# Kernel optimization log

Measured on AMD Instinct MI355X. Metric: run time of the kernel, lower is better.

The kernel has to match this reference:

```python
import jax, jax.numpy as jnp
import numpy as np

N = 40000      # nodes
E = 640000     # edges (avg degree 16)
F_IN = 15      # in_node_nf
F_EDGE = 4     # in_edge_nf
H = 128        # hidden_nf
L = 4          # n_layers
OUT = 21       # graph_dec output (hardcoded in module)


def setup_inputs() -> dict:
    key = jax.random.key(0)
    ks = jax.random.split(key, 16)
    def rn(k, shape, s=0.02):
        return jax.random.normal(k, shape, dtype=jnp.float32) * s
    e_in = 2 * H + 1 + F_EDGE   # edge_mlp input width: src,tgt,radial,edge_attr
    n_in = 2 * H + F_IN         # node_mlp input width: h, agg, node_attr(h0)
    return {
        "h0": jax.random.normal(ks[0], (N, F_IN), dtype=jnp.float32),
        "x": jax.random.normal(ks[1], (N, 3), dtype=jnp.float32),
        "edges": jax.random.randint(ks[2], (2, E), 0, N, dtype=jnp.int32),
        "edge_attr": jax.random.normal(ks[3], (E, F_EDGE), dtype=jnp.float32),
        "emb_w": rn(ks[4], (F_IN, H)), "emb_b": jnp.zeros((H,), jnp.float32),
        "ew1": rn(ks[5], (L, e_in, H)), "eb1": jnp.zeros((L, H), jnp.float32),
        "ew2": rn(ks[6], (L, H, H)), "eb2": jnp.zeros((L, H), jnp.float32),
        "nw1": rn(ks[7], (L, n_in, H)), "nb1": jnp.zeros((L, H), jnp.float32),
        "nw2": rn(ks[8], (L, H, H)), "nb2": jnp.zeros((L, H), jnp.float32),
        "dw1": rn(ks[9], (H, H)), "db1": jnp.zeros((H,), jnp.float32),
        "dw2": rn(ks[10], (H, H)), "db2": jnp.zeros((H,), jnp.float32),
        "gw1": rn(ks[11], (H, H)), "gb1": jnp.zeros((H,), jnp.float32),
        "gw2": rn(ks[12], (H, OUT)), "gb2": jnp.zeros((OUT,), jnp.float32),
    }


def reference(h0, x, edges, edge_attr, emb_w, emb_b, ew1, eb1, ew2, eb2,
              nw1, nb1, nw2, nb2, dw1, db1, dw2, db2, gw1, gb1, gw2, gb2):
    silu = jax.nn.silu
    row, col = edges[0], edges[1]
    # coord2radial (coords are constant across layers; coord_model is never called)
    cd = x[row] - x[col]                                  # [E,3]
    radial = jnp.sum(cd * cd, axis=-1, keepdims=True)     # [E,1]
    h = h0 @ emb_w + emb_b                                # [N,H]
    for i in range(L):
        # edge_model: cat(h[row], h[col], radial, edge_attr) -> MLP (act on both layers)
        ein = jnp.concatenate([h[row], h[col], radial, edge_attr], axis=-1)
        ef = silu(ein @ ew1[i] + eb1[i])
        ef = silu(ef @ ew2[i] + eb2[i])                   # [E,H]
        # node_model: scatter-sum messages to row nodes, concat, MLP, residual
        agg = jax.ops.segment_sum(ef, row, num_segments=h.shape[0])  # [N,H]
        nin = jnp.concatenate([h, agg, h0], axis=-1)
        h = h + (silu(nin @ nw1[i] + nb1[i]) @ nw2[i] + nb2[i])
    # node_dec then graph_dec (per-node prediction of 21 values)
    h = silu(h @ dw1 + db1) @ dw2 + db2
    pred = silu(h @ gw1 + gb1) @ gw2 + gb2                # [N,21]
    return pred
```

## Files before the change

### kernel.cpp

```cpp
#include <hip/hip_runtime.h>
#include <hip/hip_bf16.h>
#include <math.h>

#define N_NODES 40000
#define N_EDGES 640000
#define F_IN    15
#define HID     128
#define NLAYERS 4
#define NOUT    21

#define FLAG_BIAS 1
#define FLAG_ACC  2
#define FLAG_SILU 4

typedef __attribute__((ext_vector_type(8))) short bf16x8;
typedef __attribute__((ext_vector_type(16))) float f32x16;
typedef __attribute__((ext_vector_type(2)))  float vf2;

__device__ __forceinline__ float silu_f(float x) {
    return x * __builtin_amdgcn_rcpf(1.0f + __expf(-x));
}

__device__ __forceinline__ unsigned short f2bf(float f) {
    unsigned u = __builtin_bit_cast(unsigned, f);
    unsigned r = (u + 0x7FFFu + ((u >> 16) & 1u)) >> 16;
    return (unsigned short)r;
}
__device__ __forceinline__ float bf2f(unsigned short b) {
    return __builtin_bit_cast(float, (unsigned)b << 16);
}

__device__ __forceinline__ void split2v(vf2 v, unsigned& hi2, unsigned& lo2) {
    union { __hip_bfloat162 b; unsigned u; } ch, cl;
    ch.b = __float22bfloat162_rn(make_float2(v.x, v.y));
    vf2 h;
    h.x = __builtin_bit_cast(float, ch.u << 16);
    h.y = __builtin_bit_cast(float, ch.u & 0xFFFF0000u);
    vf2 r = v - h;
    cl.b = __float22bfloat162_rn(make_float2(r.x, r.y));
    hi2 = ch.u;
    lo2 = cl.u;
}

__device__ __forceinline__ void store_split(char* a_hi, char* a_lo, int row, int col, float v) {
    unsigned short h = f2bf(v);
    unsigned short l = f2bf(v - bf2f(h));
    int byte = (row * 256 + col * 2) ^ ((row & 7) << 4);
    *(unsigned short*)(a_hi + byte) = h;
    *(unsigned short*)(a_lo + byte) = l;
}

__global__ __launch_bounds__(256) void radial_kernel(
    const float* __restrict__ x, const int* __restrict__ erow,
    const int* __restrict__ ecol, float* __restrict__ radial)
{
    int e = blockIdx.x * 256 + threadIdx.x;
    if (e >= N_EDGES) return;
    int r = erow[e], c = ecol[e];
    float dx = x[r*3+0] - x[c*3+0];
    float dy = x[r*3+1] - x[c*3+1];
    float dz = x[r*3+2] - x[c*3+2];
    radial[e] = dx*dx + dy*dy + dz*dz;
}

__global__ __launch_bounds__(256) void hist_kernel(
    const int* __restrict__ erow, int* __restrict__ cnt)
{
    int e = blockIdx.x * 256 + threadIdx.x;
    if (e < N_EDGES) atomicAdd(&cnt[erow[e]], 1);
}

__global__ __launch_bounds__(1024) void scan_kernel(
    const int* __restrict__ cnt, int* __restrict__ rowptr)
{
    __shared__ int s[1024];
    __shared__ int carry_s;
    const int tid = threadIdx.x;
    if (tid == 0) { carry_s = 0; rowptr[0] = 0; }
    __syncthreads();
    for (int base = 0; base < N_NODES; base += 1024) {
        int i = base + tid;
        int v = (i < N_NODES) ? cnt[i] : 0;
        s[tid] = v;
        __syncthreads();
        for (int off = 1; off < 1024; off <<= 1) {
            int t = (tid >= off) ? s[tid - off] : 0;
            __syncthreads();
            s[tid] += t;
            __syncthreads();
        }
        int c = carry_s;
        if (i < N_NODES) rowptr[i + 1] = c + s[tid];
        __syncthreads();
        if (tid == 1023) carry_s = c + s[1023];
        __syncthreads();
    }
}

__global__ __launch_bounds__(256) void scatter_kernel(
    const int* __restrict__ erow, const int* __restrict__ ecol,
    const float* __restrict__ radial, const float* __restrict__ edge_attr,
    const int* __restrict__ rowptr, int* __restrict__ fill,
    int* __restrict__ srow, int* __restrict__ scol,
    float* __restrict__ srad, float* __restrict__ sea)
{
    int e = blockIdx.x * 256 + threadIdx.x;
    if (e >= N_EDGES) return;
    int r = erow[e];
    int pos = rowptr[r] + atomicAdd(&fill[r], 1);
    srow[pos] = r;
    scol[pos] = ecol[e];
    srad[pos] = radial[e];
    float4 ea = *(const float4*)&edge_attr[(size_t)e * 4];
    *(float4*)&sea[(size_t)pos * 4] = ea;
}

#define OFF_W2   0
#define OFF_W1A  65536
#define OFF_W1B  131072
#define OFF_NW1  196608
#define OFF_NW2  335872
#define OFF_DW1  401408
#define OFF_DW2  417792
#define OFF_GW1  434176
#define W_TOTAL  450560

__global__ __launch_bounds__(256) void prep_all_kernel(
    const float* __restrict__ ew1, const float* __restrict__ ew2,
    const float* __restrict__ nw1, const float* __restrict__ nw2,
    const float* __restrict__ dw1, const float* __restrict__ dw2,
    const float* __restrict__ gw1,
    unsigned short* __restrict__ hi, unsigned short* __restrict__ lo)
{
    const int T = blockIdx.y;
    int srcSel, srcOff, K, dstOff;
    if (T < 4)       { srcSel=1; srcOff=T*16384;           K=128; dstOff=OFF_W2 +T*16384; }
    else if (T < 8)  { int l=T-4;  srcSel=0; srcOff=l*33408;        K=128; dstOff=OFF_W1A+l*16384; }
    else if (T < 12) { int l=T-8;  srcSel=0; srcOff=l*33408+16384;  K=128; dstOff=OFF_W1B+l*16384; }
    else if (T < 16) { int l=T-12; srcSel=2; srcOff=l*34688;        K=271; dstOff=OFF_NW1+l*34816; }
    else if (T < 20) { int l=T-16; srcSel=3; srcOff=l*16384;        K=128; dstOff=OFF_NW2+l*16384; }
    else if (T == 20){ srcSel=4; srcOff=0; K=128; dstOff=OFF_DW1; }
    else if (T == 21){ srcSel=5; srcOff=0; K=128; dstOff=OFF_DW2; }
    else             { srcSel=6; srcOff=0; K=128; dstOff=OFF_GW1; }

    const float* src;
    switch (srcSel) {
        case 0: src = ew1; break;  case 1: src = ew2; break;
        case 2: src = nw1; break;  case 3: src = nw2; break;
        case 4: src = dw1; break;  case 5: src = dw2; break;
        default: src = gw1; break;
    }
    int K16 = (K + 15) & ~15;
    int idx = blockIdx.x * 256 + threadIdx.x;
    if (idx >= K16 * 128) return;
    int k = idx >> 7, c = idx & 127;
    float v = (k < K) ? src[srcOff + k * 128 + c] : 0.0f;
    unsigned short h = f2bf(v);
    unsigned short lw = f2bf(v - bf2f(h));
    int o = dstOff + ((k >> 3) << 10) + (c << 3) + (k & 7);
    hi[o] = h; lo[o] = lw;
}

__global__ __launch_bounds__(256) void gemm_kernel(
    const float* __restrict__ A, int lda,
    const float* __restrict__ W, int ldw,
    const float* __restrict__ bias,
    float* __restrict__ out, int ldout,
    int M, int K, int J, int flags)
{
    __shared__ float s_a[32 * 132];
    const int tid = threadIdx.x;
    const int row0 = blockIdx.x * 32;

    for (int idx = tid; idx < 32 * K; idx += 256) {
        int r = (K == 128) ? (idx >> 7) : (idx / K);
        int k = idx - r * K;
        int gr = row0 + r;
        s_a[r * 132 + k] = (gr < M) ? A[(size_t)gr * lda + k] : 0.0f;
    }
    __syncthreads();

    const int jg = tid & 31;
    const int rg = tid >> 5;
    const int j  = jg * 4;
    const int r0 = rg * 4;

    float acc[4][4] = {};

    if (j < J) {
        const bool w4ok = ((ldw & 3) == 0) && (j + 4 <= J);
        int k = 0;
        for (; k + 4 <= K; k += 4) {
            float4 av[4];
            #pragma unroll
            for (int i = 0; i < 4; i++)
                av[i] = *(const float4*)&s_a[(r0 + i) * 132 + k];
            #pragma unroll
            for (int kk = 0; kk < 4; kk++) {
                const float* wp = W + (size_t)(k + kk) * ldw + j;
                float4 w4;
                if (w4ok) {
                    w4 = *(const float4*)wp;
                } else {
                    w4.x = (j + 0 < J) ? wp[0] : 0.0f;
                    w4.y = (j + 1 < J) ? wp[1] : 0.0f;
                    w4.z = (j + 2 < J) ? wp[2] : 0.0f;
                    w4.w = (j + 3 < J) ? wp[3] : 0.0f;
                }
                #pragma unroll
                for (int i = 0; i < 4; i++) {
                    float a = ((const float*)&av[i])[kk];
                    acc[i][0] += a * w4.x;
                    acc[i][1] += a * w4.y;
                    acc[i][2] += a * w4.z;
                    acc[i][3] += a * w4.w;
                }
            }
        }
        for (; k < K; k++) {
            const float* wp = W + (size_t)k * ldw + j;
            float w0 = (j + 0 < J) ? wp[0] : 0.0f;
            float w1 = (j + 1 < J) ? wp[1] : 0.0f;
            float w2 = (j + 2 < J) ? wp[2] : 0.0f;
            float w3 = (j + 3 < J) ? wp[3] : 0.0f;
            #pragma unroll
            for (int i = 0; i < 4; i++) {
                float a = s_a[(r0 + i) * 132 + k];
                acc[i][0] += a * w0;
                acc[i][1] += a * w1;
                acc[i][2] += a * w2;
                acc[i][3] += a * w3;
            }
        }
    }

    #pragma unroll
    for (int i = 0; i < 4; i++) {
        int gr = row0 + r0 + i;
        if (gr >= M) continue;
        #pragma unroll
        for (int t = 0; t < 4; t++) {
            int jj = j + t;
            if (jj >= J) continue;
            float v = acc[i][t];
            if (flags & FLAG_BIAS) v += bias[jj];
            if (flags & FLAG_ACC)  v += out[(size_t)gr * ldout + jj];
            if (flags & FLAG_SILU) v = silu_f(v);
            out[(size_t)gr * ldout + jj] = v;
        }
    }
}

__device__ __forceinline__ void stage_a_chunk(
    char* a_hi, char* a_lo,
    const float* __restrict__ A1, int lda1, int KA1,
    const float* __restrict__ A2, int lda2, int KA,
    int kc, int row0, int lane, int w)
{
    if (kc + 128 <= KA1) {
        #pragma unroll 4
        for (int it = 0; it < 16; ++it) {
            int row = it * 4 + w;
            vf2 v = *(const vf2*)&A1[(size_t)(row0 + row) * lda1 + kc + lane * 2];
            unsigned hi2, lo2;
            split2v(v, hi2, lo2);
            int byte = (row * 256 + lane * 4) ^ ((row & 7) << 4);
            *(unsigned*)(a_hi + byte) = hi2;
            *(unsigned*)(a_lo + byte) = lo2;
        }
    } else {
        for (int it = 0; it < 16; ++it) {
            int row = it * 4 + w;
            vf2 vv;
            #pragma unroll
            for (int d = 0; d < 2; ++d) {
                int k = kc + lane * 2 + d;
                float v = 0.0f;
                if (k < KA1) v = A1[(size_t)(row0 + row) * lda1 + k];
                else if (k < KA) v = A2[(size_t)(row0 + row) * lda2 + (k - KA1)];
                vv[d] = v;
            }
            unsigned hi2, lo2;
            split2v(vv, hi2, lo2);
            int byte = (row * 256 + lane * 4) ^ ((row & 7) << 4);
            *(unsigned*)(a_hi + byte) = hi2;
            *(unsigned*)(a_lo + byte) = lo2;
        }
    }
}

__device__ __forceinline__ void mfma_chunk(
    const char* a_hi, const char* a_lo,
    const unsigned short* __restrict__ bhi, const unsigned short* __restrict__ blo,
    int kc, int nks, int lid, int khalf, int colw,
    f32x16& acc0, f32x16& acc1)
{
    const int sw0 = (lid & 7) << 4;
    for (int ks = 0; ks < nks; ++ks) {
        int ab = (lid * 256 + ks * 32 + khalf * 16) ^ sw0;
        bf16x8 ah0 = *(const bf16x8*)(a_hi + ab);
        bf16x8 al0 = *(const bf16x8*)(a_lo + ab);
        bf16x8 ah1 = *(const bf16x8*)(a_hi + ab + 8192);
        bf16x8 al1 = *(const bf16x8*)(a_lo + ab + 8192);
        int slot = (kc >> 3) + (ks << 1) + khalf;
        bf16x8 bh = *(const bf16x8*)(bhi + (slot << 10) + (colw << 3));
        bf16x8 bl = *(const bf16x8*)(blo + (slot << 10) + (colw << 3));
        acc0 = __builtin_amdgcn_mfma_f32_32x32x16_bf16(ah0, bh, acc0, 0, 0, 0);
        acc1 = __builtin_amdgcn_mfma_f32_32x32x16_bf16(ah1, bh, acc1, 0, 0, 0);
        acc0 = __builtin_amdgcn_mfma_f32_32x32x16_bf16(ah0, bl, acc0, 0, 0, 0);
        acc1 = __builtin_amdgcn_mfma_f32_32x32x16_bf16(ah1, bl, acc1, 0, 0, 0);
        acc0 = __builtin_amdgcn_mfma_f32_32x32x16_bf16(al0, bh, acc0, 0, 0, 0);
        acc1 = __builtin_amdgcn_mfma_f32_32x32x16_bf16(al1, bh, acc1, 0, 0, 0);
    }
}

__global__ __launch_bounds__(256) void mfma_gemm_kernel(
    const float* __restrict__ A1, int lda1, int KA1,
    const float* __restrict__ A2, int lda2, int KA,
    const unsigned short* __restrict__ bhi, const unsigned short* __restrict__ blo,
    const float* __restrict__ bias, float* __restrict__ out, int ldout, int flags)
{
    __shared__ char a_hi[16384];
    __shared__ char a_lo[16384];

    const int tid   = threadIdx.x;
    const int lane  = tid & 63;
    const int w     = tid >> 6;
    const int row0  = blockIdx.x * 64;
    const int lid   = lane & 31;
    const int khalf = lane >> 5;
    const int colw  = (w << 5) + lid;
    const int K16   = (KA + 15) & ~15;

    f32x16 acc0, acc1;
    #pragma unroll
    for (int i = 0; i < 16; ++i) { acc0[i] = 0.f; acc1[i] = 0.f; }

    for (int kc = 0; kc < K16; kc += 128) {
        int CK = K16 - kc; if (CK > 128) CK = 128;
        __syncthreads();
        stage_a_chunk(a_hi, a_lo, A1, lda1, KA1, A2, lda2, KA, kc, row0, lane, w);
        __syncthreads();
        mfma_chunk(a_hi, a_lo, bhi, blo, kc, CK >> 4, lid, khalf, colw, acc0, acc1);
    }

    float bcol = (flags & FLAG_BIAS) ? bias[colw] : 0.0f;
    #pragma unroll
    for (int reg = 0; reg < 16; ++reg) {
        int rr = (reg & 3) + ((reg >> 2) << 3) + (khalf << 2);
        float v0 = acc0[reg] + bcol;
        float v1 = acc1[reg] + bcol;
        float* p0 = &out[(size_t)(row0 + rr) * ldout + colw];
        float* p1 = &out[(size_t)(row0 + rr + 32) * ldout + colw];
        if (flags & FLAG_ACC) { v0 += *p0; v1 += *p1; }
        if (flags & FLAG_SILU) { v0 = silu_f(v0); v1 = silu_f(v1); }
        *p0 = v0; *p1 = v1;
    }
}

__global__ __launch_bounds__(256) void mfma_proj_kernel(
    const float* __restrict__ hb,
    const unsigned short* __restrict__ wahi, const unsigned short* __restrict__ walo,
    const unsigned short* __restrict__ wbhi, const unsigned short* __restrict__ wblo,
    const float* __restrict__ b1, float* __restrict__ P, float* __restrict__ hbw)
{
    __shared__ char a_hi[16384];
    __shared__ char a_lo[16384];

    const int tid   = threadIdx.x;
    const int lane  = tid & 63;
    const int w     = tid >> 6;
    const int row0  = blockIdx.x * 64;
    const int lid   = lane & 31;
    const int khalf = lane >> 5;
    const int colw  = (w << 5) + lid;

    stage_a_chunk(a_hi, a_lo, hb, 256, 128, nullptr, 0, 128, 0, row0, lane, w);
    __syncthreads();

    f32x16 aA0, aA1, aB0, aB1;
    #pragma unroll
    for (int i = 0; i < 16; ++i) { aA0[i]=0.f; aA1[i]=0.f; aB0[i]=0.f; aB1[i]=0.f; }

    const int sw0 = (lid & 7) << 4;
    #pragma unroll 2
    for (int ks = 0; ks < 8; ++ks) {
        int ab = (lid * 256 + ks * 32 + khalf * 16) ^ sw0;
        bf16x8 ah0 = *(const bf16x8*)(a_hi + ab);
        bf16x8 al0 = *(const bf16x8*)(a_lo + ab);
        bf16x8 ah1 = *(const bf16x8*)(a_hi + ab + 8192);
        bf16x8 al1 = *(const bf16x8*)(a_lo + ab + 8192);
        int slot = (ks << 1) + khalf;
        bf16x8 bah = *(const bf16x8*)(wahi + (slot << 10) + (colw << 3));
        bf16x8 bal = *(const bf16x8*)(walo + (slot << 10) + (colw << 3));
        bf16x8 bbh = *(const bf16x8*)(wbhi + (slot << 10) + (colw << 3));
        bf16x8 bbl = *(const bf16x8*)(wblo + (slot << 10) + (colw << 3));
        aA0 = __builtin_amdgcn_mfma_f32_32x32x16_bf16(ah0, bah, aA0, 0, 0, 0);
        aA1 = __builtin_amdgcn_mfma_f32_32x32x16_bf16(ah1, bah, aA1, 0, 0, 0);
        aB0 = __builtin_amdgcn_mfma_f32_32x32x16_bf16(ah0, bbh, aB0, 0, 0, 0);
        aB1 = __builtin_amdgcn_mfma_f32_32x32x16_bf16(ah1, bbh, aB1, 0, 0, 0);
        aA0 = __builtin_amdgcn_mfma_f32_32x32x16_bf16(ah0, bal, aA0, 0, 0, 0);
        aA1 = __builtin_amdgcn_mfma_f32_32x32x16_bf16(ah1, bal, aA1, 0, 0, 0);
        aB0 = __builtin_amdgcn_mfma_f32_32x32x16_bf16(ah0, bbl, aB0, 0, 0, 0);
        aB1 = __builtin_amdgcn_mfma_f32_32x32x16_bf16(ah1, bbl, aB1, 0, 0, 0);
        aA0 = __builtin_amdgcn_mfma_f32_32x32x16_bf16(al0, bah, aA0, 0, 0, 0);
        aA1 = __builtin_amdgcn_mfma_f32_32x32x16_bf16(al1, bah, aA1, 0, 0, 0);
        aB0 = __builtin_amdgcn_mfma_f32_32x32x16_bf16(al0, bbh, aB0, 0, 0, 0);
        aB1 = __builtin_amdgcn_mfma_f32_32x32x16_bf16(al1, bbh, aB1, 0, 0, 0);
    }

    float bcol = b1[colw];
    #pragma unroll
    for (int reg = 0; reg < 16; ++reg) {
        int rr = (reg & 3) + ((reg >> 2) << 3) + (khalf << 2);
        size_t r0o = (size_t)(row0 + rr) * 256;
        size_t r1o = (size_t)(row0 + rr + 32) * 256;
        P[r0o + colw]       = aA0[reg] + bcol;
        P[r1o + colw]       = aA1[reg] + bcol;
        P[r0o + 128 + colw] = aB0[reg];
        P[r1o + 128 + colw] = aB1[reg];
        hbw[r0o + 128 + colw] = 0.0f;
        hbw[r1o + 128 + colw] = 0.0f;
    }
}

__global__ __launch_bounds__(256) void mfma_chain2_kernel(
    const float* __restrict__ A1, int lda1, int KA1,
    const float* __restrict__ A2, int lda2, int KA,
    const unsigned short* __restrict__ w1hi, const unsigned short* __restrict__ w1lo,
    const float* __restrict__ bias1, int flags1,
    const unsigned short* __restrict__ w2hi, const unsigned short* __restrict__ w2lo,
    const float* __restrict__ bias2, int flags2,
    float* __restrict__ out, int ldout)
{
    __shared__ char a_hi[16384];
    __shared__ char a_lo[16384];

    const int tid   = threadIdx.x;
    const int lane  = tid & 63;
    const int w     = tid >> 6;
    const int row0  = blockIdx.x * 64;
    const int lid   = lane & 31;
    const int khalf = lane >> 5;
    const int colw  = (w << 5) + lid;
    const int K16   = (KA + 15) & ~15;

    f32x16 acc0, acc1;
    #pragma unroll
    for (int i = 0; i < 16; ++i) { acc0[i] = 0.f; acc1[i] = 0.f; }

    for (int kc = 0; kc < K16; kc += 128) {
        int CK = K16 - kc; if (CK > 128) CK = 128;
        __syncthreads();
        stage_a_chunk(a_hi, a_lo, A1, lda1, KA1, A2, lda2, KA, kc, row0, lane, w);
        __syncthreads();
        mfma_chunk(a_hi, a_lo, w1hi, w1lo, kc, CK >> 4, lid, khalf, colw, acc0, acc1);
    }

    __syncthreads();
    {
        float b1c = (flags1 & FLAG_BIAS) ? bias1[colw] : 0.0f;
        #pragma unroll
        for (int reg = 0; reg < 16; ++reg) {
            int rr = (reg & 3) + ((reg >> 2) << 3) + (khalf << 2);
            float v0 = acc0[reg] + b1c;
            float v1 = acc1[reg] + b1c;
            if (flags1 & FLAG_SILU) { v0 = silu_f(v0); v1 = silu_f(v1); }
            store_split(a_hi, a_lo, rr, colw, v0);
            store_split(a_hi, a_lo, rr + 32, colw, v1);
        }
    }
    __syncthreads();

    #pragma unroll
    for (int i = 0; i < 16; ++i) { acc0[i] = 0.f; acc1[i] = 0.f; }
    mfma_chunk(a_hi, a_lo, w2hi, w2lo, 0, 8, lid, khalf, colw, acc0, acc1);

    float bcol = (flags2 & FLAG_BIAS) ? bias2[colw] : 0.0f;
    #pragma unroll
    for (int reg = 0; reg < 16; ++reg) {
        int rr = (reg & 3) + ((reg >> 2) << 3) + (khalf << 2);
        float v0 = acc0[reg] + bcol;
        float v1 = acc1[reg] + bcol;
        float* p0 = &out[(size_t)(row0 + rr) * ldout + colw];
        float* p1 = &out[(size_t)(row0 + rr + 32) * ldout + colw];
        if (flags2 & FLAG_ACC) { v0 += *p0; v1 += *p1; }
        if (flags2 & FLAG_SILU) { v0 = silu_f(v0); v1 = silu_f(v1); }
        *p0 = v0; *p1 = v1;
    }
}

__global__ __launch_bounds__(256) void edge_kernel(
    const float* __restrict__ P,
    const int* __restrict__ srow, const int* __restrict__ scol,
    const float* __restrict__ srad, const float* __restrict__ sea,
    const unsigned short* __restrict__ w2tb_hi,
    const unsigned short* __restrict__ w2tb_lo,
    const float* __restrict__ b2,
    const float* __restrict__ wr, const float* __restrict__ we,
    float* __restrict__ hb)
{
    __shared__ char smem[64 * 132 * 4];
    __shared__ int   s_row[64];
    __shared__ int   s_col[64];
    __shared__ float s_rad[64];
    __shared__ float s_ea4[64 * 4];
    __shared__ int   s_segstart[66];
    __shared__ int   s_nseg;

    char* a_hi = smem;
    char* a_lo = smem + 16384;
    float* s_ef = (float*)smem;

    const int tid  = threadIdx.x;
    const int lane = tid & 63;
    const int w    = tid >> 6;
    const int p0   = blockIdx.x * 64;

    if (tid < 64) {
        s_row[tid] = srow[p0 + tid];
        s_col[tid] = scol[p0 + tid];
        s_rad[tid] = srad[p0 + tid];
        *(float4*)&s_ea4[tid * 4] = *(const float4*)&sea[(size_t)(p0 + tid) * 4];
    }
    __syncthreads();

    if (tid < 64) {
        bool flag = (tid == 0) || (s_row[tid] != s_row[tid - 1]);
        unsigned long long mask = __ballot(flag);
        int idx = __popcll(mask & ((1ull << tid) - 1));
        if (flag) s_segstart[idx] = tid;
        if (tid == 0) { int ns = __popcll(mask); s_nseg = ns; s_segstart[ns] = 64; }
    }

    const int k2 = lane * 2;
    const vf2 wrv = *(const vf2*)&wr[k2];
    const vf2 wa0 = *(const vf2*)&we[0 * 128 + k2];
    const vf2 wa1 = *(const vf2*)&we[1 * 128 + k2];
    const vf2 wa2 = *(const vf2*)&we[2 * 128 + k2];
    const vf2 wa3 = *(const vf2*)&we[3 * 128 + k2];
    #pragma unroll 4
    for (int it = 0; it < 16; ++it) {
        int et = it * 4 + w;
        int r = s_row[et], c = s_col[et];
        float rad = s_rad[et];
        float4 ea = *(const float4*)&s_ea4[et * 4];
        vf2 ps = *(const vf2*)&P[(size_t)r * 256 + k2];
        vf2 pt = *(const vf2*)&P[(size_t)c * 256 + 128 + k2];
        vf2 pre = ps + pt;
        pre += rad * wrv;
        pre += ea.x * wa0;
        pre += ea.y * wa1;
        pre += ea.z * wa2;
        pre += ea.w * wa3;
        vf2 sl;
        sl.x = silu_f(pre.x);
        sl.y = silu_f(pre.y);
        unsigned hi2, lo2;
        split2v(sl, hi2, lo2);
        int byte = (et * 256 + lane * 4) ^ ((et & 7) << 4);
        *(unsigned*)(a_hi + byte) = hi2;
        *(unsigned*)(a_lo + byte) = lo2;
    }
    __syncthreads();

    const int lid   = lane & 31;
    const int khalf = lane >> 5;
    const int colw  = (w << 5) + lid;
    f32x16 acc0, acc1;
    #pragma unroll
    for (int i = 0; i < 16; ++i) { acc0[i] = 0.f; acc1[i] = 0.f; }
    mfma_chunk(a_hi, a_lo, w2tb_hi, w2tb_lo, 0, 8, lid, khalf, colw, acc0, acc1);
    __syncthreads();

    float bcol = b2[colw];
    #pragma unroll
    for (int reg = 0; reg < 16; ++reg) {
        int rr = (reg & 3) + ((reg >> 2) << 3) + (khalf << 2);
        s_ef[rr * 132 + colw]        = silu_f(acc0[reg] + bcol);
        s_ef[(rr + 32) * 132 + colw] = silu_f(acc1[reg] + bcol);
    }
    __syncthreads();

    const int jg = tid & 31, rg = tid >> 5;
    const int j = jg * 4;
    const int nseg = s_nseg;
    for (int s = rg; s < nseg; s += 8) {
        int sp0 = s_segstart[s], sp1 = s_segstart[s + 1];
        float v0 = 0.f, v1 = 0.f, v2 = 0.f, v3 = 0.f;
        for (int p = sp0; p < sp1; ++p) {
            float4 q = *(const float4*)&s_ef[p * 132 + j];
            v0 += q.x; v1 += q.y; v2 += q.z; v3 += q.w;
        }
        int rowId = s_row[sp0];
        bool interior = true;
        if (sp0 == 0 && p0 > 0 && srow[p0 - 1] == rowId) interior = false;
        if (sp1 == 64 && p0 + 64 < N_EDGES && srow[p0 + 64] == rowId) interior = false;
        float* dst = &hb[(size_t)rowId * 256 + 128 + j];
        if (interior) {
            *(float4*)dst = make_float4(v0, v1, v2, v3);
        } else {
            atomicAdd(&dst[0], v0); atomicAdd(&dst[1], v1);
            atomicAdd(&dst[2], v2); atomicAdd(&dst[3], v3);
        }
    }
}

extern "C" void kernel_launch(void* const* d_in, const int* in_sizes, int n_in,
                              void* d_out, int out_size, void* d_ws, size_t ws_size,
                              hipStream_t stream)
{
    const float* h0       = (const float*)d_in[0];
    const float* x        = (const float*)d_in[1];
    const int*   edges    = (const int*)  d_in[2];
    const float* edge_attr= (const float*)d_in[3];
    const float* emb_w    = (const float*)d_in[4];
    const float* emb_b    = (const float*)d_in[5];
    const float* ew1      = (const float*)d_in[6];
    const float* eb1      = (const float*)d_in[7];
    const float* ew2      = (const float*)d_in[8];
    const float* eb2      = (const float*)d_in[9];
    const float* nw1      = (const float*)d_in[10];
    const float* nb1      = (const float*)d_in[11];
    const float* nw2      = (const float*)d_in[12];
    const float* nb2      = (const float*)d_in[13];
    const float* dw1      = (const float*)d_in[14];
    const float* db1      = (const float*)d_in[15];
    const float* dw2      = (const float*)d_in[16];
    const float* db2      = (const float*)d_in[17];
    const float* gw1      = (const float*)d_in[18];
    const float* gb1      = (const float*)d_in[19];
    const float* gw2      = (const float*)d_in[20];
    const float* gb2      = (const float*)d_in[21];
    float* out = (float*)d_out;

    char* ws = (char*)d_ws;
    const size_t SZ_HB = (size_t)N_NODES * 256 * 4;
    const size_t SZ_T  = (size_t)N_NODES * HID * 4;
    const size_t SZ_E  = (size_t)N_EDGES * 4;
    float* hb     = (float*)(ws);
    float* P      = (float*)(ws + SZ_HB);
    float* tmp1   = (float*)(ws + SZ_HB * 2);
    char*  base   = ws + SZ_HB * 2 + SZ_T;
    float* radial = (float*)(base);
    int*   s_row  = (int*)  (base + SZ_E);
    int*   s_col  = (int*)  (base + SZ_E * 2);
    float* s_rad  = (float*)(base + SZ_E * 3);
    float* s_ea   = (float*)(base + SZ_E * 4);
    int*   rowptr = (int*)  (base + SZ_E * 8);
    int*   cnt    = (int*)  (base + SZ_E * 8 + (N_NODES + 64) * 4);
    unsigned short* w_hi = (unsigned short*)radial;
    unsigned short* w_lo = w_hi + W_TOTAL;

    const int* erow = edges;
    const int* ecol = edges + N_EDGES;

    radial_kernel<<<N_EDGES / 256, 256, 0, stream>>>(x, erow, ecol, radial);

    hipMemsetAsync(cnt, 0, N_NODES * 4, stream);
    hist_kernel<<<N_EDGES / 256, 256, 0, stream>>>(erow, cnt);
    scan_kernel<<<1, 1024, 0, stream>>>(cnt, rowptr);
    hipMemsetAsync(cnt, 0, N_NODES * 4, stream);
    scatter_kernel<<<N_EDGES / 256, 256, 0, stream>>>(
        erow, ecol, radial, edge_attr, rowptr, cnt, s_row, s_col, s_rad, s_ea);

    prep_all_kernel<<<dim3(136, 23), 256, 0, stream>>>(
        ew1, ew2, nw1, nw2, dw1, dw2, gw1, w_hi, w_lo);

    gemm_kernel<<<(N_NODES + 31) / 32, 256, 0, stream>>>(
        h0, F_IN, emb_w, HID, emb_b, hb, 256, N_NODES, F_IN, HID, FLAG_BIAS);

    for (int l = 0; l < NLAYERS; ++l) {
        const float* W1   = ew1 + (size_t)l * 261 * 128;
        const float* b1   = eb1 + l * 128;
        const float* b2v  = eb2 + l * 128;
        const float* nb1v = nb1 + l * 128;
        const float* nb2v = nb2 + l * 128;

        mfma_proj_kernel<<<625, 256, 0, stream>>>(
            hb,
            w_hi + OFF_W1A + l * 16384, w_lo + OFF_W1A + l * 16384,
            w_hi + OFF_W1B + l * 16384, w_lo + OFF_W1B + l * 16384,
            b1, P, hb);

        edge_kernel<<<N_EDGES / 64, 256, 0, stream>>>(
            P, s_row, s_col, s_rad, s_ea,
            w_hi + OFF_W2 + (size_t)l * 16384, w_lo + OFF_W2 + (size_t)l * 16384,
            b2v, W1 + 256 * 128, W1 + 257 * 128, hb);

        mfma_chain2_kernel<<<625, 256, 0, stream>>>(
            hb, 256, 256, h0, F_IN, 271,
            w_hi + OFF_NW1 + l * 34816, w_lo + OFF_NW1 + l * 34816,
            nb1v, FLAG_BIAS | FLAG_SILU,
            w_hi + OFF_NW2 + l * 16384, w_lo + OFF_NW2 + l * 16384,
            nb2v, FLAG_BIAS | FLAG_ACC,
            hb, 256);
    }

    mfma_chain2_kernel<<<625, 256, 0, stream>>>(
        hb, 256, 128, nullptr, 0, 128,
        w_hi + OFF_DW1, w_lo + OFF_DW1, db1, FLAG_BIAS | FLAG_SILU,
        w_hi + OFF_DW2, w_lo + OFF_DW2, db2, FLAG_BIAS,
        P, 128);
    mfma_gemm_kernel<<<625, 256, 0, stream>>>(
        P, 128, 128, nullptr, 0, 128, w_hi + OFF_GW1, w_lo + OFF_GW1,
        gb1, tmp1, HID, FLAG_BIAS | FLAG_SILU);
    gemm_kernel<<<(N_NODES + 31) / 32, 256, 0, stream>>>(
        tmp1, HID, gw2, NOUT, gb2, out, NOUT, N_NODES, HID, NOUT, FLAG_BIAS);
}
```

Baseline: 953.4 us.

## Fuse node MLP with next-layer edge projection and merge decoder GEMM chain

Each node-update kernel now also computes the next layer's per-node edge projections (P) from the updated h held in shared memory, and zeroes the aggregation buffer, which removes a separate projection launch and a re-read of h per layer. The decoder's three 128x128 GEMMs are fused into one kernel that keeps intermediates in LDS. The edge kernel preloads its W2 fragments into registers and reads edge metadata straight from global memory instead of staging it in LDS. The cost is much higher register pressure (four accumulators in the fused node kernel, 16 weight fragments in the edge kernel), which may reduce occupancy.

Result: slower. 1.371 ms (+43.8%).

```diff
diff --git a/kernel.cpp b/kernel.cpp
--- a/kernel.cpp
+++ b/kernel.cpp
@@ -314,50 +314,6 @@
     }
 }
 
-__global__ __launch_bounds__(256) void mfma_gemm_kernel(
-    const float* __restrict__ A1, int lda1, int KA1,
-    const float* __restrict__ A2, int lda2, int KA,
-    const unsigned short* __restrict__ bhi, const unsigned short* __restrict__ blo,
-    const float* __restrict__ bias, float* __restrict__ out, int ldout, int flags)
-{
-    __shared__ char a_hi[16384];
-    __shared__ char a_lo[16384];
-
-    const int tid   = threadIdx.x;
-    const int lane  = tid & 63;
-    const int w     = tid >> 6;
-    const int row0  = blockIdx.x * 64;
-    const int lid   = lane & 31;
-    const int khalf = lane >> 5;
-    const int colw  = (w << 5) + lid;
-    const int K16   = (KA + 15) & ~15;
-
-    f32x16 acc0, acc1;
-    #pragma unroll
-    for (int i = 0; i < 16; ++i) { acc0[i] = 0.f; acc1[i] = 0.f; }
-
-    for (int kc = 0; kc < K16; kc += 128) {
-        int CK = K16 - kc; if (CK > 128) CK = 128;
-        __syncthreads();
-        stage_a_chunk(a_hi, a_lo, A1, lda1, KA1, A2, lda2, KA, kc, row0, lane, w);
-        __syncthreads();
-        mfma_chunk(a_hi, a_lo, bhi, blo, kc, CK >> 4, lid, khalf, colw, acc0, acc1);
-    }
-
-    float bcol = (flags & FLAG_BIAS) ? bias[colw] : 0.0f;
-    #pragma unroll
-    for (int reg = 0; reg < 16; ++reg) {
-        int rr = (reg & 3) + ((reg >> 2) << 3) + (khalf << 2);
-        float v0 = acc0[reg] + bcol;
-        float v1 = acc1[reg] + bcol;
-        float* p0 = &out[(size_t)(row0 + rr) * ldout + colw];
-        float* p1 = &out[(size_t)(row0 + rr + 32) * ldout + colw];
-        if (flags & FLAG_ACC) { v0 += *p0; v1 += *p1; }
-        if (flags & FLAG_SILU) { v0 = silu_f(v0); v1 = silu_f(v1); }
-        *p0 = v0; *p1 = v1;
-    }
-}
-
 __global__ __launch_bounds__(256) void mfma_proj_kernel(
     const float* __restrict__ hb,
     const unsigned short* __restrict__ wahi, const unsigned short* __restrict__ walo,
@@ -490,6 +446,182 @@
     }
 }
 
+__global__ __launch_bounds__(256) void chain3_node_kernel(
+    const float* __restrict__ hb, const float* __restrict__ h0,
+    const unsigned short* __restrict__ w1hi, const unsigned short* __restrict__ w1lo,
+    const float* __restrict__ nb1v,
+    const unsigned short* __restrict__ w2hi, const unsigned short* __restrict__ w2lo,
+    const float* __restrict__ nb2v,
+    const unsigned short* __restrict__ pahi, const unsigned short* __restrict__ palo,
+    const unsigned short* __restrict__ pbhi, const unsigned short* __restrict__ pblo,
+    const float* __restrict__ b1n,
+    float* __restrict__ hbw, float* __restrict__ P)
+{
+    __shared__ char a_hi[16384];
+    __shared__ char a_lo[16384];
+
+    const int tid   = threadIdx.x;
+    const int lane  = tid & 63;
+    const int w     = tid >> 6;
+    const int row0  = blockIdx.x * 64;
+    const int lid   = lane & 31;
+    const int khalf = lane >> 5;
+    const int colw  = (w << 5) + lid;
+
+    f32x16 acc0, acc1;
+    #pragma unroll
+    for (int i = 0; i < 16; ++i) { acc0[i] = 0.f; acc1[i] = 0.f; }
+    for (int kc = 0; kc < 272; kc += 128) {
+        int CK = 272 - kc; if (CK > 128) CK = 128;
+        __syncthreads();
+        stage_a_chunk(a_hi, a_lo, hb, 256, 256, h0, F_IN, 271, kc, row0, lane, w);
+        __syncthreads();
+        mfma_chunk(a_hi, a_lo, w1hi, w1lo, kc, CK >> 4, lid, khalf, colw, acc0, acc1);
+    }
+    __syncthreads();
+    {
+        float b1c = nb1v[colw];
+        #pragma unroll
+        for (int reg = 0; reg < 16; ++reg) {
+            int rr = (reg & 3) + ((reg >> 2) << 3) + (khalf << 2);
+            store_split(a_hi, a_lo, rr, colw, silu_f(acc0[reg] + b1c));
+            store_split(a_hi, a_lo, rr + 32, colw, silu_f(acc1[reg] + b1c));
+        }
+    }
+    __syncthreads();
+
+    #pragma unroll
+    for (int i = 0; i < 16; ++i) { acc0[i] = 0.f; acc1[i] = 0.f; }
+    mfma_chunk(a_hi, a_lo, w2hi, w2lo, 0, 8, lid, khalf, colw, acc0, acc1);
+    __syncthreads();
+    {
+        float b2c = nb2v[colw];
+        #pragma unroll
+        for (int reg = 0; reg < 16; ++reg) {
+            int rr = (reg & 3) + ((reg >> 2) << 3) + (khalf << 2);
+            size_t r0o = (size_t)(row0 + rr) * 256;
+            size_t r1o = (size_t)(row0 + rr + 32) * 256;
+            float v0 = acc0[reg] + b2c + hbw[r0o + colw];
+            float v1 = acc1[reg] + b2c + hbw[r1o + colw];
+            hbw[r0o + colw] = v0;
+            hbw[r1o + colw] = v1;
+            hbw[r0o + 128 + colw] = 0.0f;
+            hbw[r1o + 128 + colw] = 0.0f;
+            store_split(a_hi, a_lo, rr, colw, v0);
+            store_split(a_hi, a_lo, rr + 32, colw, v1);
+        }
+    }
+    __syncthreads();
+
+    f32x16 aA0, aA1, aB0, aB1;
+    #pragma unroll
+    for (int i = 0; i < 16; ++i) { aA0[i]=0.f; aA1[i]=0.f; aB0[i]=0.f; aB1[i]=0.f; }
+    const int sw0 = (lid & 7) << 4;
+    #pragma unroll 2
+    for (int ks = 0; ks < 8; ++ks) {
+        int ab = (lid * 256 + ks * 32 + khalf * 16) ^ sw0;
+        bf16x8 ah0 = *(const bf16x8*)(a_hi + ab);
+        bf16x8 al0 = *(const bf16x8*)(a_lo + ab);
+        bf16x8 ah1 = *(const bf16x8*)(a_hi + ab + 8192);
+        bf16x8 al1 = *(const bf16x8*)(a_lo + ab + 8192);
+        int slot = (ks << 1) + khalf;
+        bf16x8 bah = *(const bf16x8*)(pahi + (slot << 10) + (colw << 3));
+        bf16x8 bal = *(const bf16x8*)(palo + (slot << 10) + (colw << 3));
+        bf16x8 bbh = *(const bf16x8*)(pbhi + (slot << 10) + (colw << 3));
+        bf16x8 bbl = *(const bf16x8*)(pblo + (slot << 10) + (colw << 3));
+        aA0 = __builtin_amdgcn_mfma_f32_32x32x16_bf16(ah0, bah, aA0, 0, 0, 0);
+        aA1 = __builtin_amdgcn_mfma_f32_32x32x16_bf16(ah1, bah, aA1, 0, 0, 0);
+        aB0 = __builtin_amdgcn_mfma_f32_32x32x16_bf16(ah0, bbh, aB0, 0, 0, 0);
+        aB1 = __builtin_amdgcn_mfma_f32_32x32x16_bf16(ah1, bbh, aB1, 0, 0, 0);
+        aA0 = __builtin_amdgcn_mfma_f32_32x32x16_bf16(ah0, bal, aA0, 0, 0, 0);
+        aA1 = __builtin_amdgcn_mfma_f32_32x32x16_bf16(ah1, bal, aA1, 0, 0, 0);
+        aB0 = __builtin_amdgcn_mfma_f32_32x32x16_bf16(ah0, bbl, aB0, 0, 0, 0);
+        aB1 = __builtin_amdgcn_mfma_f32_32x32x16_bf16(ah1, bbl, aB1, 0, 0, 0);
+        aA0 = __builtin_amdgcn_mfma_f32_32x32x16_bf16(al0, bah, aA0, 0, 0, 0);
+        aA1 = __builtin_amdgcn_mfma_f32_32x32x16_bf16(al1, bah, aA1, 0, 0, 0);
+        aB0 = __builtin_amdgcn_mfma_f32_32x32x16_bf16(al0, bbh, aB0, 0, 0, 0);
+        aB1 = __builtin_amdgcn_mfma_f32_32x32x16_bf16(al1, bbh, aB1, 0, 0, 0);
+    }
+    float bcol = b1n[colw];
+    #pragma unroll
+    for (int reg = 0; reg < 16; ++reg) {
+        int rr = (reg & 3) + ((reg >> 2) << 3) + (khalf << 2);
+        size_t r0o = (size_t)(row0 + rr) * 256;
+        size_t r1o = (size_t)(row0 + rr + 32) * 256;
+        P[r0o + colw]       = aA0[reg] + bcol;
+        P[r1o + colw]       = aA1[reg] + bcol;
+        P[r0o + 128 + colw] = aB0[reg];
+        P[r1o + 128 + colw] = aB1[reg];
+    }
+}
+
+__global__ __launch_bounds__(256) void chain3_dec_kernel(
+    const float* __restrict__ hb,
+    const unsigned short* __restrict__ w1hi, const unsigned short* __restrict__ w1lo,
+    const float* __restrict__ b1,
+    const unsigned short* __restrict__ w2hi, const unsigned short* __restrict__ w2lo,
+    const float* __restrict__ b2,
+    const unsigned short* __restrict__ w3hi, const unsigned short* __restrict__ w3lo,
+    const float* __restrict__ b3,
+    float* __restrict__ out)
+{
+    __shared__ char a_hi[16384];
+    __shared__ char a_lo[16384];
+
+    const int tid   = threadIdx.x;
+    const int lane  = tid & 63;
+    const int w     = tid >> 6;
+    const int row0  = blockIdx.x * 64;
+    const int lid   = lane & 31;
+    const int khalf = lane >> 5;
+    const int colw  = (w << 5) + lid;
+
+    f32x16 acc0, acc1;
+
+    #pragma unroll
+    for (int i = 0; i < 16; ++i) { acc0[i] = 0.f; acc1[i] = 0.f; }
+    stage_a_chunk(a_hi, a_lo, hb, 256, 128, nullptr, 0, 128, 0, row0, lane, w);
+    __syncthreads();
+    mfma_chunk(a_hi, a_lo, w1hi, w1lo, 0, 8, lid, khalf, colw, acc0, acc1);
+    __syncthreads();
+    {
+        float bc = b1[colw];
+        #pragma unroll
+        for (int reg = 0; reg < 16; ++reg) {
+            int rr = (reg & 3) + ((reg >> 2) << 3) + (khalf << 2);
+            store_split(a_hi, a_lo, rr, colw, silu_f(acc0[reg] + bc));
+            store_split(a_hi, a_lo, rr + 32, colw, silu_f(acc1[reg] + bc));
+        }
+    }
+    __syncthreads();
+
+    #pragma unroll
+    for (int i = 0; i < 16; ++i) { acc0[i] = 0.f; acc1[i] = 0.f; }
+    mfma_chunk(a_hi, a_lo, w2hi, w2lo, 0, 8, lid, khalf, colw, acc0, acc1);
+    __syncthreads();
+    {
+        float bc = b2[colw];
+        #pragma unroll
+        for (int reg = 0; reg < 16; ++reg) {
+            int rr = (reg & 3) + ((reg >> 2) << 3) + (khalf << 2);
+            store_split(a_hi, a_lo, rr, colw, acc0[reg] + bc);
+            store_split(a_hi, a_lo, rr + 32, colw, acc1[reg] + bc);
+        }
+    }
+    __syncthreads();
+
+    #pragma unroll
+    for (int i = 0; i < 16; ++i) { acc0[i] = 0.f; acc1[i] = 0.f; }
+    mfma_chunk(a_hi, a_lo, w3hi, w3lo, 0, 8, lid, khalf, colw, acc0, acc1);
+    float bc = b3[colw];
+    #pragma unroll
+    for (int reg = 0; reg < 16; ++reg) {
+        int rr = (reg & 3) + ((reg >> 2) << 3) + (khalf << 2);
+        out[(size_t)(row0 + rr) * HID + colw]      = silu_f(acc0[reg] + bc);
+        out[(size_t)(row0 + rr + 32) * HID + colw] = silu_f(acc1[reg] + bc);
+    }
+}
+
 __global__ __launch_bounds__(256) void edge_kernel(
     const float* __restrict__ P,
     const int* __restrict__ srow, const int* __restrict__ scol,
@@ -502,9 +634,6 @@
 {
     __shared__ char smem[64 * 132 * 4];
     __shared__ int   s_row[64];
-    __shared__ int   s_col[64];
-    __shared__ float s_rad[64];
-    __shared__ float s_ea4[64 * 4];
     __shared__ int   s_segstart[66];
     __shared__ int   s_nseg;
 
@@ -517,12 +646,19 @@
     const int w    = tid >> 6;
     const int p0   = blockIdx.x * 64;
 
-    if (tid < 64) {
-        s_row[tid] = srow[p0 + tid];
-        s_col[tid] = scol[p0 + tid];
-        s_rad[tid] = srad[p0 + tid];
-        *(float4*)&s_ea4[tid * 4] = *(const float4*)&sea[(size_t)(p0 + tid) * 4];
-    }
+    const int lid   = lane & 31;
+    const int khalf = lane >> 5;
+    const int colw  = (w << 5) + lid;
+
+    bf16x8 bhv[8], blv[8];
+    #pragma unroll
+    for (int ks = 0; ks < 8; ++ks) {
+        int slot = (ks << 1) + khalf;
+        bhv[ks] = *(const bf16x8*)(w2tb_hi + (slot << 10) + (colw << 3));
+        blv[ks] = *(const bf16x8*)(w2tb_lo + (slot << 10) + (colw << 3));
+    }
+
+    if (tid < 64) s_row[tid] = srow[p0 + tid];
     __syncthreads();
 
     if (tid < 64) {
@@ -542,9 +678,10 @@
     #pragma unroll 4
     for (int it = 0; it < 16; ++it) {
         int et = it * 4 + w;
-        int r = s_row[et], c = s_col[et];
-        float rad = s_rad[et];
-        float4 ea = *(const float4*)&s_ea4[et * 4];
+        int p  = p0 + et;
+        int r = srow[p], c = scol[p];
+        float rad = srad[p];
+        float4 ea = *(const float4*)&sea[(size_t)p * 4];
         vf2 ps = *(const vf2*)&P[(size_t)r * 256 + k2];
         vf2 pt = *(const vf2*)&P[(size_t)c * 256 + 128 + k2];
         vf2 pre = ps + pt;
@@ -564,13 +701,24 @@
     }
     __syncthreads();
 
-    const int lid   = lane & 31;
-    const int khalf = lane >> 5;
-    const int colw  = (w << 5) + lid;
     f32x16 acc0, acc1;
     #pragma unroll
     for (int i = 0; i < 16; ++i) { acc0[i] = 0.f; acc1[i] = 0.f; }
-    mfma_chunk(a_hi, a_lo, w2tb_hi, w2tb_lo, 0, 8, lid, khalf, colw, acc0, acc1);
+    const int sw0 = (lid & 7) << 4;
+    #pragma unroll
+    for (int ks = 0; ks < 8; ++ks) {
+        int ab = (lid * 256 + ks * 32 + khalf * 16) ^ sw0;
+        bf16x8 ah0 = *(const bf16x8*)(a_hi + ab);
+        bf16x8 al0 = *(const bf16x8*)(a_lo + ab);
+        bf16x8 ah1 = *(const bf16x8*)(a_hi + ab + 8192);
+        bf16x8 al1 = *(const bf16x8*)(a_lo + ab + 8192);
+        acc0 = __builtin_amdgcn_mfma_f32_32x32x16_bf16(ah0, bhv[ks], acc0, 0, 0, 0);
+        acc1 = __builtin_amdgcn_mfma_f32_32x32x16_bf16(ah1, bhv[ks], acc1, 0, 0, 0);
+        acc0 = __builtin_amdgcn_mfma_f32_32x32x16_bf16(ah0, blv[ks], acc0, 0, 0, 0);
+        acc1 = __builtin_amdgcn_mfma_f32_32x32x16_bf16(ah1, blv[ks], acc1, 0, 0, 0);
+        acc0 = __builtin_amdgcn_mfma_f32_32x32x16_bf16(al0, bhv[ks], acc0, 0, 0, 0);
+        acc1 = __builtin_amdgcn_mfma_f32_32x32x16_bf16(al1, bhv[ks], acc1, 0, 0, 0);
+    }
     __syncthreads();
 
     float bcol = b2[colw];
@@ -670,41 +818,47 @@
     gemm_kernel<<<(N_NODES + 31) / 32, 256, 0, stream>>>(
         h0, F_IN, emb_w, HID, emb_b, hb, 256, N_NODES, F_IN, HID, FLAG_BIAS);
 
+    mfma_proj_kernel<<<625, 256, 0, stream>>>(
+        hb, w_hi + OFF_W1A, w_lo + OFF_W1A, w_hi + OFF_W1B, w_lo + OFF_W1B,
+        eb1, P, hb);
+
     for (int l = 0; l < NLAYERS; ++l) {
         const float* W1   = ew1 + (size_t)l * 261 * 128;
-        const float* b1   = eb1 + l * 128;
         const float* b2v  = eb2 + l * 128;
         const float* nb1v = nb1 + l * 128;
         const float* nb2v = nb2 + l * 128;
-
-        mfma_proj_kernel<<<625, 256, 0, stream>>>(
-            hb,
-            w_hi + OFF_W1A + l * 16384, w_lo + OFF_W1A + l * 16384,
-            w_hi + OFF_W1B + l * 16384, w_lo + OFF_W1B + l * 16384,
-            b1, P, hb);
 
         edge_kernel<<<N_EDGES / 64, 256, 0, stream>>>(
             P, s_row, s_col, s_rad, s_ea,
             w_hi + OFF_W2 + (size_t)l * 16384, w_lo + OFF_W2 + (size_t)l * 16384,
             b2v, W1 + 256 * 128, W1 + 257 * 128, hb);
 
-        mfma_chain2_kernel<<<625, 256, 0, stream>>>(
-            hb, 256, 256, h0, F_IN, 271,
-            w_hi + OFF_NW1 + l * 34816, w_lo + OFF_NW1 + l * 34816,
-            nb1v, FLAG_BIAS | FLAG_SILU,
-            w_hi + OFF_NW2 + l * 16384, w_lo + OFF_NW2 + l * 16384,
-            nb2v, FLAG_BIAS | FLAG_ACC,
-            hb, 256);
-    }
-
-    mfma_chain2_kernel<<<625, 256, 0, stream>>>(
-        hb, 256, 128, nullptr, 0, 128,
-        w_hi + OFF_DW1, w_lo + OFF_DW1, db1, FLAG_BIAS | FLAG_SILU,
-        w_hi + OFF_DW2, w_lo + OFF_DW2, db2, FLAG_BIAS,
-        P, 128);
-    mfma_gemm_kernel<<<625, 256, 0, stream>>>(
-        P, 128, 128, nullptr, 0, 128, w_hi + OFF_GW1, w_lo + OFF_GW1,
-        gb1, tmp1, HID, FLAG_BIAS | FLAG_SILU);
+        if (l < NLAYERS - 1) {
+            chain3_node_kernel<<<625, 256, 0, stream>>>(
+                hb, h0,
+                w_hi + OFF_NW1 + l * 34816, w_lo + OFF_NW1 + l * 34816, nb1v,
+                w_hi + OFF_NW2 + l * 16384, w_lo + OFF_NW2 + l * 16384, nb2v,
+                w_hi + OFF_W1A + (l + 1) * 16384, w_lo + OFF_W1A + (l + 1) * 16384,
+                w_hi + OFF_W1B + (l + 1) * 16384, w_lo + OFF_W1B + (l + 1) * 16384,
+                eb1 + (l + 1) * 128,
+                hb, P);
+        } else {
+            mfma_chain2_kernel<<<625, 256, 0, stream>>>(
+                hb, 256, 256, h0, F_IN, 271,
+                w_hi + OFF_NW1 + l * 34816, w_lo + OFF_NW1 + l * 34816,
+                nb1v, FLAG_BIAS | FLAG_SILU,
+                w_hi + OFF_NW2 + l * 16384, w_lo + OFF_NW2 + l * 16384,
+                nb2v, FLAG_BIAS | FLAG_ACC,
+                hb, 256);
+        }
+    }
+
+    chain3_dec_kernel<<<625, 256, 0, stream>>>(
+        hb,
+        w_hi + OFF_DW1, w_lo + OFF_DW1, db1,
+        w_hi + OFF_DW2, w_lo + OFF_DW2, db2,
+        w_hi + OFF_GW1, w_lo + OFF_GW1, gb1,
+        tmp1);
     gemm_kernel<<<(N_NODES + 31) / 32, 256, 0, stream>>>(
         tmp1, HID, gw2, NOUT, gb2, out, NOUT, N_NODES, HID, NOUT, FLAG_BIAS);
 }
```
